# Optimization experiments

Hardware: AMD Instinct MI355X
Metric: run time of the kernel (lower is better)

The kernel has to match this reference:

```python
import jax, jax.numpy as jnp
import numpy as np

B, T, C = 2, 2048, 1024
H = 16
D = C // H  # head_size = 64
EPS = 1e-5


def setup_inputs() -> dict:
    key = jax.random.key(0)
    ks = jax.random.split(key, 16)
    s = lambda fan_in: fan_in ** -0.5
    return {
        "x": jax.random.normal(ks[0], (B, T, C), jnp.float32),
        "Wq": jax.random.normal(ks[1], (H, C, D), jnp.float32) * s(C),
        "Wk": jax.random.normal(ks[2], (H, C, D), jnp.float32) * s(C),
        "Wv": jax.random.normal(ks[3], (H, C, D), jnp.float32) * s(C),
        "Wproj": jax.random.normal(ks[4], (C, C), jnp.float32) * s(C),
        "bproj": jnp.zeros((C,), jnp.float32),
        "W1": jax.random.normal(ks[5], (C, 4 * C), jnp.float32) * s(C),
        "b1": jnp.zeros((4 * C,), jnp.float32),
        "W2": jax.random.normal(ks[6], (4 * C, C), jnp.float32) * s(4 * C),
        "b2": jnp.zeros((C,), jnp.float32),
        "ln1_g": jnp.ones((C,), jnp.float32),
        "ln1_b": jnp.zeros((C,), jnp.float32),
        "ln2_g": jnp.ones((C,), jnp.float32),
        "ln2_b": jnp.zeros((C,), jnp.float32),
    }


def _layernorm(x, g, b):
    mu = jnp.mean(x, axis=-1, keepdims=True)
    var = jnp.mean(jnp.square(x - mu), axis=-1, keepdims=True)
    return (x - mu) * jax.lax.rsqrt(var + EPS) * g + b


def _block(x, Wq, Wk, Wv, Wproj, bproj, W1, b1, W2, b2,
           ln1_g, ln1_b, ln2_g, ln2_b):
    # --- multi-head causal self-attention (pre-LN) ---
    h = _layernorm(x, ln1_g, ln1_b)
    q = jnp.einsum("btc,hcd->bhtd", h, Wq)
    k = jnp.einsum("btc,hcd->bhtd", h, Wk)
    v = jnp.einsum("btc,hcd->bhtd", h, Wv)
    scores = jnp.einsum("bhtd,bhsd->bhts", q, k) * (D ** -0.5)  # [B,H,T,T]
    causal = jnp.tril(jnp.ones((T, T), bool))
    scores = jnp.where(causal, scores, -jnp.inf)
    att = jax.nn.softmax(scores, axis=-1)
    out = jnp.einsum("bhts,bhsd->bhtd", att, v)  # [B,H,T,D]
    out = out.transpose(0, 2, 1, 3).reshape(B, T, H * D)  # concat heads
    x = x + out @ Wproj + bproj
    # --- feed-forward ---
    h2 = _layernorm(x, ln2_g, ln2_b)
    ff = jax.nn.relu(h2 @ W1 + b1) @ W2 + b2
    return x + ff


def reference(x, Wq, Wk, Wv, Wproj, bproj, W1, b1, W2, b2,
              ln1_g, ln1_b, ln2_g, ln2_b):
    return _block(x, Wq, Wk, Wv, Wproj, bproj, W1, b1, W2, b2,
                  ln1_g, ln1_b, ln2_g, ln2_b)
```

## Files before the change

### kernel.cpp

```cpp
#include <hip/hip_runtime.h>

typedef __bf16 bf16x8 __attribute__((ext_vector_type(8)));
typedef float  f32x4  __attribute__((ext_vector_type(4)));

union U8 { bf16x8 v; __bf16 e[8]; unsigned short u[8]; };

__device__ __forceinline__ unsigned short f2bf(float f) {
  unsigned int u = __float_as_uint(f);
  unsigned int r = (u + 0x7FFFu + ((u >> 16) & 1u)) >> 16;
  return (unsigned short)r;
}

__device__ __forceinline__ void async16(const void* g, void* l) {
  __builtin_amdgcn_global_load_lds(
      (__attribute__((address_space(1))) void*)(g),
      (__attribute__((address_space(3))) void*)(l), 16, 0, 0);
}

__device__ __forceinline__ void block_barrier() {
  asm volatile("" ::: "memory");
  __builtin_amdgcn_sched_barrier(0);
  __builtin_amdgcn_s_barrier();
  __builtin_amdgcn_sched_barrier(0);
  asm volatile("" ::: "memory");
}

__global__ __launch_bounds__(256) void transpose_w(
    const float* __restrict__ in, unsigned short* __restrict__ out,
    int R, int Cc) {
  __shared__ float tile[32][33];
  const int batch = blockIdx.z;
  const float* ip = in + (size_t)batch * R * Cc;
  unsigned short* op = out + (size_t)batch * R * Cc;
  const int c0 = blockIdx.x * 32, r0 = blockIdx.y * 32;
  const int tx = threadIdx.x, ty = threadIdx.y;
#pragma unroll
  for (int i = 0; i < 32; i += 8)
    tile[ty + i][tx] = ip[(size_t)(r0 + ty + i) * Cc + c0 + tx];
  __syncthreads();
#pragma unroll
  for (int i = 0; i < 32; i += 8)
    op[(size_t)(c0 + ty + i) * R + r0 + tx] = f2bf(tile[tx][ty + i]);
}

__global__ __launch_bounds__(256) void ln_kernel(
    const float* __restrict__ x, const float* __restrict__ g,
    const float* __restrict__ bta, unsigned short* __restrict__ out) {
  const int C = 1024;
  const int row = blockIdx.x, tid = threadIdx.x;
  const float4 v = ((const float4*)(x + (size_t)row * C))[tid];
  float s  = v.x + v.y + v.z + v.w;
  float ss = v.x * v.x + v.y * v.y + v.z * v.z + v.w * v.w;
#pragma unroll
  for (int off = 32; off > 0; off >>= 1) {
    s  += __shfl_down(s, off);
    ss += __shfl_down(ss, off);
  }
  __shared__ float r0[4], r1[4];
  const int wave = tid >> 6, lane = tid & 63;
  if (lane == 0) { r0[wave] = s; r1[wave] = ss; }
  __syncthreads();
  s  = r0[0] + r0[1] + r0[2] + r0[3];
  ss = r1[0] + r1[1] + r1[2] + r1[3];
  const float mu   = s * (1.0f / C);
  const float var  = ss * (1.0f / C) - mu * mu;
  const float rstd = rsqrtf(var + 1e-5f);
  const float4 gv = ((const float4*)g)[tid];
  const float4 bv = ((const float4*)bta)[tid];
  ushort4 o;
  o.x = f2bf((v.x - mu) * rstd * gv.x + bv.x);
  o.y = f2bf((v.y - mu) * rstd * gv.y + bv.y);
  o.z = f2bf((v.z - mu) * rstd * gv.z + bv.z);
  o.w = f2bf((v.w - mu) * rstd * gv.w + bv.w);
  ((ushort4*)(out + (size_t)row * C))[tid] = o;
}

__global__ __launch_bounds__(256, 2) void gemm_lat2(
    const unsigned short* __restrict__ A, const unsigned short* __restrict__ BT,
    float* __restrict__ Cout, const float* __restrict__ bias,
    const float* __restrict__ resid, int M, int N, int K) {
  __shared__ __align__(16) unsigned short As[3][8192];
  __shared__ __align__(16) unsigned short Bs[3][4096];
  const int tid = threadIdx.x;
  const int lane = tid & 63, wave = tid >> 6;
  const int wm = wave >> 1, wn = wave & 1;
  const int lr = lane & 15, lg = lane >> 4;

  const int nwg = gridDim.x;
  const int cpx = nwg >> 3;
  const int swz = ((int)blockIdx.x & 7) * cpx + ((int)blockIdx.x >> 3);
  const int Nt = N >> 6;
  const int g4 = swz / (4 * Nt);
  const int rem = swz - g4 * 4 * Nt;
  const int m0 = (g4 * 4 + (rem & 3)) << 7;
  const int n0 = (rem >> 2) << 6;

  const int srow = tid >> 3;
  const int sc = ((tid & 7) ^ (srow & 7)) << 3;
  const unsigned short* Ag = A + (size_t)(m0 + srow) * K + sc;
  const unsigned short* Bg = BT + (size_t)(n0 + srow) * K + sc;
  const size_t rskip = (size_t)32 * K;

  f32x4 acc[4][2] = {};
  const int nkt = K >> 6;

#define STG(T, B)                                                          \
  {                                                                        \
    const int kt_ = (T) << 6;                                              \
    _Pragma("unroll")                                                      \
    for (int j = 0; j < 4; ++j)                                            \
      async16(Ag + kt_ + (size_t)j * rskip, &As[B][j * 2048 + tid * 8]);   \
    async16(Bg + kt_, &Bs[B][tid * 8]);                                    \
    async16(Bg + kt_ + rskip, &Bs[B][2048 + tid * 8]);                     \
  }

  STG(0, 0);
  STG(1, 1);

  for (int t = 0; t < nkt; ++t) {
    const int buf = t % 3;
    if (t + 1 < nkt) asm volatile("s_waitcnt vmcnt(6)" ::: "memory");
    else             asm volatile("s_waitcnt vmcnt(0)" ::: "memory");
    block_barrier();
    if (t + 2 < nkt) {
      int sb = buf + 2; if (sb >= 3) sb -= 3;
      STG(t + 2, sb);
    }
#pragma unroll
    for (int kh = 0; kh < 2; ++kh) {
      const int kc = ((kh * 4 + lg) ^ (lr & 7)) << 3;
      bf16x8 afr[4], bfr[2];
#pragma unroll
      for (int fm = 0; fm < 4; fm++)
        afr[fm] = *(const bf16x8*)&As[buf][(wm * 64 + fm * 16 + lr) * 64 + kc];
#pragma unroll
      for (int fn = 0; fn < 2; fn++)
        bfr[fn] = *(const bf16x8*)&Bs[buf][(wn * 32 + fn * 16 + lr) * 64 + kc];
#pragma unroll
      for (int fm = 0; fm < 4; fm++)
#pragma unroll
        for (int fn = 0; fn < 2; fn++)
          acc[fm][fn] = __builtin_amdgcn_mfma_f32_16x16x32_bf16(
              afr[fm], bfr[fn], acc[fm][fn], 0, 0, 0);
    }
  }
#undef STG

#pragma unroll
  for (int fn = 0; fn < 2; fn++) {
    const int col = n0 + wn * 32 + fn * 16 + lr;
    const float bv = bias[col];
#pragma unroll
    for (int fm = 0; fm < 4; fm++) {
      const int row0 = m0 + wm * 64 + fm * 16 + lg * 4;
#pragma unroll
      for (int r = 0; r < 4; r++) {
        const size_t idx = (size_t)(row0 + r) * N + col;
        Cout[idx] = acc[fm][fn][r] + bv + resid[idx];
      }
    }
  }
}

template <int EPI>
__global__ __launch_bounds__(512, 2) void gemm8p(
    const unsigned short* __restrict__ A, const unsigned short* __restrict__ BT,
    void* __restrict__ Cout, void* __restrict__ Cout2,
    const float* __restrict__ bias, int M, int N, int K) {
  __shared__ __align__(16) unsigned short As[2][2][8192];
  __shared__ __align__(16) unsigned short Bs[2][2][8192];
  const int tid = threadIdx.x;
  const int lane = tid & 63;
  const int wave = tid >> 6;
  const int wm = wave >> 2, wn = wave & 3;
  const int lr = lane & 15, lg = lane >> 4;

  const int nwg = gridDim.x;
  const int cpx = nwg >> 3;
  const int swz = ((int)blockIdx.x & 7) * cpx + ((int)blockIdx.x >> 3);
  const int Nt = N >> 8;
  const int g4 = swz / (4 * Nt);
  const int rem = swz - g4 * 4 * Nt;
  const int m0 = (g4 * 4 + (rem & 3)) << 8;
  const int n0 = (rem >> 2) << 8;

  const int srow = tid >> 2;
  const int scg = ((tid & 3) ^ ((srow >> 1) & 3)) << 3;
  const unsigned short* Ag = A + (size_t)(m0 + srow) * K + scg;
  const unsigned short* Bg = BT + (size_t)(n0 + srow) * K + scg;
  const size_t rskip = (size_t)128 * K;
  const int l8 = tid * 8;

  const int kch = (lg ^ ((lr >> 1) & 3)) << 3;

  f32x4 acc[8][4] = {};
  bf16x8 afr[4], bfr[4];
  const int nkt = K >> 6;

  async16(Ag, &As[0][0][l8]);            async16(Ag + rskip, &As[0][0][l8 + 4096]);
  async16(Bg, &Bs[0][0][l8]);            async16(Bg + rskip, &Bs[0][0][l8 + 4096]);
  async16(Ag + 32, &As[0][1][l8]);       async16(Ag + 32 + rskip, &As[0][1][l8 + 4096]);
  async16(Bg + 32, &Bs[0][1][l8]);       async16(Bg + 32 + rskip, &Bs[0][1][l8 + 4096]);
  async16(Ag + 64, &As[1][0][l8]);       async16(Ag + 64 + rskip, &As[1][0][l8 + 4096]);
  async16(Bg + 64, &Bs[1][0][l8]);       async16(Bg + 64 + rskip, &Bs[1][0][l8 + 4096]);
  asm volatile("s_waitcnt vmcnt(4)" ::: "memory");
  block_barrier();

  for (int t = 0; t < nkt; ++t) {
    const int buf = t & 1, nbuf = buf ^ 1;
    const int kt1 = (t + 1) << 6, kt2 = (t + 2) << 6;
    const bool s1 = (t + 1 < nkt), s2 = (t + 2 < nkt);

#pragma unroll
    for (int fm = 0; fm < 4; fm++)
      afr[fm] = *(const bf16x8*)&As[buf][0][(wm * 128 + fm * 16 + lr) * 32 + kch];
#pragma unroll
    for (int fn = 0; fn < 4; fn++)
      bfr[fn] = *(const bf16x8*)&Bs[buf][0][(wn * 64 + fn * 16 + lr) * 32 + kch];
    if (s1) {
      async16(Ag + kt1 + 32, &As[nbuf][1][l8]);
      async16(Ag + kt1 + 32 + rskip, &As[nbuf][1][l8 + 4096]);
    }
    block_barrier();
    __builtin_amdgcn_s_setprio(1);
#pragma unroll
    for (int fm = 0; fm < 4; fm++)
#pragma unroll
      for (int fn = 0; fn < 4; fn++)
        acc[fm][fn] = __builtin_amdgcn_mfma_f32_16x16x32_bf16(afr[fm], bfr[fn], acc[fm][fn], 0, 0, 0);
    __builtin_amdgcn_s_setprio(0);
    block_barrier();

#pragma unroll
    for (int fm = 0; fm < 4; fm++)
      afr[fm] = *(const bf16x8*)&As[buf][0][(wm * 128 + 64 + fm * 16 + lr) * 32 + kch];
    if (s1) {
      async16(Bg + kt1 + 32, &Bs[nbuf][1][l8]);
      async16(Bg + kt1 + 32 + rskip, &Bs[nbuf][1][l8 + 4096]);
    }
    block_barrier();
    __builtin_amdgcn_s_setprio(1);
#pragma unroll
    for (int fm = 0; fm < 4; fm++)
#pragma unroll
      for (int fn = 0; fn < 4; fn++)
        acc[4 + fm][fn] = __builtin_amdgcn_mfma_f32_16x16x32_bf16(afr[fm], bfr[fn], acc[4 + fm][fn], 0, 0, 0);
    __builtin_amdgcn_s_setprio(0);
    block_barrier();

#pragma unroll
    for (int fm = 0; fm < 4; fm++)
      afr[fm] = *(const bf16x8*)&As[buf][1][(wm * 128 + fm * 16 + lr) * 32 + kch];
#pragma unroll
    for (int fn = 0; fn < 4; fn++)
      bfr[fn] = *(const bf16x8*)&Bs[buf][1][(wn * 64 + fn * 16 + lr) * 32 + kch];
    if (s2) {
      async16(Ag + kt2, &As[buf][0][l8]);
      async16(Ag + kt2 + rskip, &As[buf][0][l8 + 4096]);
    }
    block_barrier();
    __builtin_amdgcn_s_setprio(1);
#pragma unroll
    for (int fm = 0; fm < 4; fm++)
#pragma unroll
      for (int fn = 0; fn < 4; fn++)
        acc[fm][fn] = __builtin_amdgcn_mfma_f32_16x16x32_bf16(afr[fm], bfr[fn], acc[fm][fn], 0, 0, 0);
    __builtin_amdgcn_s_setprio(0);
    block_barrier();

#pragma unroll
    for (int fm = 0; fm < 4; fm++)
      afr[fm] = *(const bf16x8*)&As[buf][1][(wm * 128 + 64 + fm * 16 + lr) * 32 + kch];
    if (s2) {
      async16(Bg + kt2, &Bs[buf][0][l8]);
      async16(Bg + kt2 + rskip, &Bs[buf][0][l8 + 4096]);
    }
    block_barrier();
    __builtin_amdgcn_s_setprio(1);
#pragma unroll
    for (int fm = 0; fm < 4; fm++)
#pragma unroll
      for (int fn = 0; fn < 4; fn++)
        acc[4 + fm][fn] = __builtin_amdgcn_mfma_f32_16x16x32_bf16(afr[fm], bfr[fn], acc[4 + fm][fn], 0, 0, 0);
    __builtin_amdgcn_s_setprio(0);
    if (s2) asm volatile("s_waitcnt vmcnt(4)" ::: "memory");
    else    asm volatile("s_waitcnt vmcnt(0)" ::: "memory");
    block_barrier();
  }

#pragma unroll
  for (int fn = 0; fn < 4; fn++) {
    const int col = n0 + wn * 64 + fn * 16 + lr;
    float bv = 0.0f;
    if (EPI == 2) bv = bias[col];
#pragma unroll
    for (int fm = 0; fm < 8; fm++) {
      const int row0 = m0 + wm * 128 + fm * 16 + lg * 4;
      if (EPI == 2) {
#pragma unroll
        for (int r = 0; r < 4; r++)
          ((unsigned short*)Cout)[(size_t)(row0 + r) * N + col] =
              f2bf(fmaxf(acc[fm][fn][r] + bv, 0.0f));
      } else {
        if (col < 2048) {
#pragma unroll
          for (int r = 0; r < 4; r++)
            ((unsigned short*)Cout)[(size_t)(row0 + r) * 2048 + col] =
                f2bf(acc[fm][fn][r]);
        } else {
          ushort4 ov;
          ov.x = f2bf(acc[fm][fn][0]);
          ov.y = f2bf(acc[fm][fn][1]);
          ov.z = f2bf(acc[fm][fn][2]);
          ov.w = f2bf(acc[fm][fn][3]);
          *(ushort4*)((unsigned short*)Cout2 + (size_t)(col - 2048) * 4096 + row0) = ov;
        }
      }
    }
  }
}

__global__ __launch_bounds__(256) void attn_kernel(
    const unsigned short* __restrict__ qk, const unsigned short* __restrict__ vT,
    unsigned short* __restrict__ o) {
  const int T = 2048, C = 1024, QKS = 2048;
  const int tid = threadIdx.x;
  const int wave = tid >> 6, lane = tid & 63;
  const int lr = lane & 15, lg = lane >> 4;
  const int b = blockIdx.y >> 4, hh = blockIdx.y & 15;
  const size_t rowb = (size_t)b * T * QKS;
  const int qcol = hh * 64;
  const int kcol = 1024 + hh * 64;
  const int vrow0 = hh * 64;
  const size_t bT = (size_t)b * T;
  const int swe = (lr & 7) << 3;

  __shared__ __align__(16) unsigned short Ks[2][64 * 64];
  __shared__ __align__(16) unsigned short Vs[2][64 * 64];
  __shared__ __align__(16) unsigned short Ps[4][16][72];

  const int rw = tid >> 3;
  const int c8 = ((tid & 7) ^ (rw & 7)) << 3;

#pragma unroll 1
  for (int pass = 0; pass < 2; ++pass) {
    const int qt = (pass == 0) ? (int)blockIdx.x : (31 - (int)blockIdx.x);
    const int qbase = qt * 64 + wave * 16;
    const int trow = qbase + lr;

    U8 qf[2];
#pragma unroll
    for (int j = 0; j < 2; j++)
      qf[j].v = *(const bf16x8*)(qk + rowb + (size_t)trow * QKS + qcol + j * 32 + lg * 8);
    asm volatile("s_waitcnt vmcnt(0)" ::: "memory");

    async16(qk + rowb + (size_t)rw * QKS + kcol + c8, Ks[0] + tid * 8);
    async16(qk + rowb + (size_t)(32 + rw) * QKS + kcol + c8, Ks[0] + 2048 + tid * 8);
    async16(vT + (size_t)(vrow0 + rw) * 4096 + bT + c8, Vs[0] + tid * 8);
    async16(vT + (size_t)(vrow0 + 32 + rw) * 4096 + bT + c8, Vs[0] + 2048 + tid * 8);

    f32x4 oa[4] = {};
    float mrun = -1e30f, lsum = 0.0f;
    int cur = 0;

    for (int sb = 0; sb <= qt; ++sb) {
      if (sb < qt) {
        const int s1 = (sb + 1) * 64;
        const int nb = cur ^ 1;
        async16(qk + rowb + (size_t)(s1 + rw) * QKS + kcol + c8, Ks[nb] + tid * 8);
        async16(qk + rowb + (size_t)(s1 + 32 + rw) * QKS + kcol + c8, Ks[nb] + 2048 + tid * 8);
        async16(vT + (size_t)(vrow0 + rw) * 4096 + bT + s1 + c8, Vs[nb] + tid * 8);
        async16(vT + (size_t)(vrow0 + 32 + rw) * 4096 + bT + s1 + c8, Vs[nb] + 2048 + tid * 8);
        asm volatile("s_waitcnt vmcnt(4)" ::: "memory");
      } else {
        asm volatile("s_waitcnt vmcnt(0)" ::: "memory");
      }
      block_barrier();

      const unsigned short* Kc = Ks[cur];
      const unsigned short* Vc = Vs[cur];
      const int s0 = sb * 64;

      f32x4 sa[4] = {};
#pragma unroll
      for (int j = 0; j < 2; j++) {
#pragma unroll
        for (int mf = 0; mf < 4; mf++) {
          U8 kf;
          kf.v = *(const bf16x8*)(Kc + (mf * 16 + lr) * 64 + ((j * 32 + lg * 8) ^ swe));
          sa[mf] = __builtin_amdgcn_mfma_f32_16x16x32_bf16(kf.v, qf[j].v, sa[mf], 0, 0, 0);
        }
      }
      float sv[16];
#pragma unroll
      for (int mf = 0; mf < 4; mf++)
#pragma unroll
        for (int r = 0; r < 4; r++) sv[mf * 4 + r] = sa[mf][r] * 0.125f;

      if (sb == qt) {
#pragma unroll
        for (int mf = 0; mf < 4; mf++)
#pragma unroll
          for (int r = 0; r < 4; r++)
            if (s0 + mf * 16 + lg * 4 + r > trow) sv[mf * 4 + r] = -1e30f;
      }

      float tm = sv[0];
#pragma unroll
      for (int i = 1; i < 16; i++) tm = fmaxf(tm, sv[i]);
      tm = fmaxf(tm, __shfl_xor(tm, 16));
      tm = fmaxf(tm, __shfl_xor(tm, 32));

      if (!__all(tm <= mrun + 8.0f)) {
        const float mn = fmaxf(mrun, tm);
        const float corr = __expf(mrun - mn);
        lsum *= corr;
#pragma unroll
        for (int c = 0; c < 4; c++)
#pragma unroll
          for (int r = 0; r < 4; r++) oa[c][r] *= corr;
        mrun = mn;
      }

      float rs = 0.0f;
#pragma unroll
      for (int i = 0; i < 16; i++) {
        sv[i] = __expf(sv[i] - mrun);
        rs += sv[i];
      }
      rs += __shfl_xor(rs, 16);
      rs += __shfl_xor(rs, 32);
      lsum += rs;

#pragma unroll
      for (int mf = 0; mf < 4; mf++) {
        ushort4 w;
        w.x = f2bf(sv[mf * 4 + 0]);
        w.y = f2bf(sv[mf * 4 + 1]);
        w.z = f2bf(sv[mf * 4 + 2]);
        w.w = f2bf(sv[mf * 4 + 3]);
        *(ushort4*)&Ps[wave][lr][mf * 16 + lg * 4] = w;
      }
      asm volatile("" ::: "memory");
      U8 pb[2];
      pb[0].v = *(const bf16x8*)&Ps[wave][lr][lg * 8];
      pb[1].v = *(const bf16x8*)&Ps[wave][lr][32 + lg * 8];
      asm volatile("" ::: "memory");

#pragma unroll
      for (int c = 0; c < 4; c++) {
#pragma unroll
        for (int ks = 0; ks < 2; ks++) {
          U8 vf;
          vf.v = *(const bf16x8*)(Vc + (c * 16 + lr) * 64 + ((ks * 32 + lg * 8) ^ swe));
          oa[c] = __builtin_amdgcn_mfma_f32_16x16x32_bf16(vf.v, pb[ks].v, oa[c], 0, 0, 0);
        }
      }

      block_barrier();
      cur ^= 1;
    }

    const float inv = 1.0f / lsum;
#pragma unroll
    for (int c = 0; c < 4; c++) {
      ushort4 ov;
      ov.x = f2bf(oa[c][0] * inv);
      ov.y = f2bf(oa[c][1] * inv);
      ov.z = f2bf(oa[c][2] * inv);
      ov.w = f2bf(oa[c][3] * inv);
      *(ushort4*)(o + (size_t)(bT + trow) * C + hh * 64 + c * 16 + lg * 4) = ov;
    }
  }
}

extern "C" void kernel_launch(void* const* d_in, const int* in_sizes, int n_in,
                              void* d_out, int out_size, void* d_ws, size_t ws_size,
                              hipStream_t stream) {
  (void)in_sizes; (void)n_in; (void)out_size; (void)ws_size;
  const int T = 2048, C = 1024, M = 2 * T, C4 = 4 * C;

  const float* x     = (const float*)d_in[0];
  const float* Wq    = (const float*)d_in[1];
  const float* Wk    = (const float*)d_in[2];
  const float* Wv    = (const float*)d_in[3];
  const float* Wproj = (const float*)d_in[4];
  const float* bproj = (const float*)d_in[5];
  const float* W1    = (const float*)d_in[6];
  const float* b1    = (const float*)d_in[7];
  const float* W2    = (const float*)d_in[8];
  const float* b2    = (const float*)d_in[9];
  const float* ln1g  = (const float*)d_in[10];
  const float* ln1b  = (const float*)d_in[11];
  const float* ln2g  = (const float*)d_in[12];
  const float* ln2b  = (const float*)d_in[13];
  float* out = (float*)d_out;

  char* ws = (char*)d_ws;
  const size_t MBy = (size_t)1 << 20;
  unsigned short* WqkvT = (unsigned short*)(ws + 0 * MBy);
  unsigned short* WqT = WqkvT;
  unsigned short* WkT = WqkvT + 1024 * 1024;
  unsigned short* WvT = WqkvT + 2048 * 1024;
  unsigned short* WpT = (unsigned short*)(ws + 6 * MBy);
  unsigned short* W1T = (unsigned short*)(ws + 8 * MBy);
  unsigned short* W2T = (unsigned short*)(ws + 16 * MBy);
  unsigned short* h   = (unsigned short*)(ws + 24 * MBy);
  unsigned short* qkb = (unsigned short*)(ws + 32 * MBy);
  unsigned short* vTb = (unsigned short*)(ws + 48 * MBy);
  unsigned short* att = (unsigned short*)(ws + 56 * MBy);
  float*          x1  = (float*)(ws + 64 * MBy);
  unsigned short* h2  = att;
  unsigned short* ff1 = h;

  const dim3 tb(32, 8);
  transpose_w<<<dim3(2, 32, 16), tb, 0, stream>>>(Wq, WqT, 1024, 64);
  transpose_w<<<dim3(2, 32, 16), tb, 0, stream>>>(Wk, WkT, 1024, 64);
  transpose_w<<<dim3(2, 32, 16), tb, 0, stream>>>(Wv, WvT, 1024, 64);
  transpose_w<<<dim3(32, 32, 1), tb, 0, stream>>>(Wproj, WpT, 1024, 1024);
  transpose_w<<<dim3(128, 32, 1), tb, 0, stream>>>(W1, W1T, 1024, 4096);
  transpose_w<<<dim3(32, 128, 1), tb, 0, stream>>>(W2, W2T, 4096, 1024);

  ln_kernel<<<M, 256, 0, stream>>>(x, ln1g, ln1b, h);

  gemm8p<4><<<192, 512, 0, stream>>>(h, WqkvT, qkb, vTb, nullptr, M, 3072, C);

  attn_kernel<<<dim3(16, 32), 256, 0, stream>>>(qkb, vTb, att);

  gemm_lat2<<<512, 256, 0, stream>>>(att, WpT, x1, bproj, x, M, C, C);

  ln_kernel<<<M, 256, 0, stream>>>(x1, ln2g, ln2b, h2);

  gemm8p<2><<<256, 512, 0, stream>>>(h2, W1T, ff1, nullptr, b1, M, C4, C);

  gemm_lat2<<<512, 256, 0, stream>>>(ff1, W2T, out, b2, x1, M, C, C4);
}
```

Before: 252.2 us.

## Replace LDS-staged GEMM with direct global-to-register double-buffered loads

The projection and FFN2 GEMM kernel stops staging A/B tiles through LDS with async loads and barriers. Each wave now loads its MFMA fragments straight from global memory into registers, using two register buffers so the loads for the next k-tile overlap the MFMAs on the current one. This removes the LDS traffic and block barriers, but each wave now fetches its own operand fragments with no sharing inside the workgroup. It also uses narrower, less coalesced global accesses and relies on L2/L1 to absorb the redundant reads.

```diff
diff --git a/kernel.cpp b/kernel.cpp
--- a/kernel.cpp
+++ b/kernel.cpp
@@ -75,12 +75,10 @@
   ((ushort4*)(out + (size_t)row * C))[tid] = o;
 }
 
-__global__ __launch_bounds__(256, 2) void gemm_lat2(
+__global__ __launch_bounds__(256, 2) void gemm_reg(
     const unsigned short* __restrict__ A, const unsigned short* __restrict__ BT,
     float* __restrict__ Cout, const float* __restrict__ bias,
     const float* __restrict__ resid, int M, int N, int K) {
-  __shared__ __align__(16) unsigned short As[3][8192];
-  __shared__ __align__(16) unsigned short Bs[3][4096];
   const int tid = threadIdx.x;
   const int lane = tid & 63, wave = tid >> 6;
   const int wm = wave >> 1, wn = wave & 1;
@@ -95,56 +93,72 @@
   const int m0 = (g4 * 4 + (rem & 3)) << 7;
   const int n0 = (rem >> 2) << 6;
 
-  const int srow = tid >> 3;
-  const int sc = ((tid & 7) ^ (srow & 7)) << 3;
-  const unsigned short* Ag = A + (size_t)(m0 + srow) * K + sc;
-  const unsigned short* Bg = BT + (size_t)(n0 + srow) * K + sc;
-  const size_t rskip = (size_t)32 * K;
-
+  const unsigned short* pa0 = A + (size_t)(m0 + wm * 64 +  0 + lr) * K + lg * 8;
+  const unsigned short* pa1 = A + (size_t)(m0 + wm * 64 + 16 + lr) * K + lg * 8;
+  const unsigned short* pa2 = A + (size_t)(m0 + wm * 64 + 32 + lr) * K + lg * 8;
+  const unsigned short* pa3 = A + (size_t)(m0 + wm * 64 + 48 + lr) * K + lg * 8;
+  const unsigned short* pb0 = BT + (size_t)(n0 + wn * 32 +  0 + lr) * K + lg * 8;
+  const unsigned short* pb1 = BT + (size_t)(n0 + wn * 32 + 16 + lr) * K + lg * 8;
+
+  bf16x8 a0[2][4], b0[2][2], a1[2][4], b1[2][2];
   f32x4 acc[4][2] = {};
-  const int nkt = K >> 6;
-
-#define STG(T, B)                                                          \
-  {                                                                        \
-    const int kt_ = (T) << 6;                                              \
-    _Pragma("unroll")                                                      \
-    for (int j = 0; j < 4; ++j)                                            \
-      async16(Ag + kt_ + (size_t)j * rskip, &As[B][j * 2048 + tid * 8]);   \
-    async16(Bg + kt_, &Bs[B][tid * 8]);                                    \
-    async16(Bg + kt_ + rskip, &Bs[B][2048 + tid * 8]);                     \
-  }
-
-  STG(0, 0);
-  STG(1, 1);
-
-  for (int t = 0; t < nkt; ++t) {
-    const int buf = t % 3;
-    if (t + 1 < nkt) asm volatile("s_waitcnt vmcnt(6)" ::: "memory");
-    else             asm volatile("s_waitcnt vmcnt(0)" ::: "memory");
-    block_barrier();
-    if (t + 2 < nkt) {
-      int sb = buf + 2; if (sb >= 3) sb -= 3;
-      STG(t + 2, sb);
-    }
-#pragma unroll
-    for (int kh = 0; kh < 2; ++kh) {
-      const int kc = ((kh * 4 + lg) ^ (lr & 7)) << 3;
-      bf16x8 afr[4], bfr[2];
-#pragma unroll
-      for (int fm = 0; fm < 4; fm++)
-        afr[fm] = *(const bf16x8*)&As[buf][(wm * 64 + fm * 16 + lr) * 64 + kc];
-#pragma unroll
-      for (int fn = 0; fn < 2; fn++)
-        bfr[fn] = *(const bf16x8*)&Bs[buf][(wn * 32 + fn * 16 + lr) * 64 + kc];
-#pragma unroll
-      for (int fm = 0; fm < 4; fm++)
-#pragma unroll
-        for (int fn = 0; fn < 2; fn++)
-          acc[fm][fn] = __builtin_amdgcn_mfma_f32_16x16x32_bf16(
-              afr[fm], bfr[fn], acc[fm][fn], 0, 0, 0);
-    }
-  }
-#undef STG
+
+#define LD_T0                                                     \
+  {                                                               \
+    _Pragma("unroll")                                             \
+    for (int kh = 0; kh < 2; kh++) {                              \
+      a0[kh][0] = *(const bf16x8*)(pa0 + kh * 32);                \
+      a0[kh][1] = *(const bf16x8*)(pa1 + kh * 32);                \
+      a0[kh][2] = *(const bf16x8*)(pa2 + kh * 32);                \
+      a0[kh][3] = *(const bf16x8*)(pa3 + kh * 32);                \
+      b0[kh][0] = *(const bf16x8*)(pb0 + kh * 32);                \
+      b0[kh][1] = *(const bf16x8*)(pb1 + kh * 32);                \
+    }                                                             \
+  }
+#define LD_T1                                                     \
+  {                                                               \
+    _Pragma("unroll")                                             \
+    for (int kh = 0; kh < 2; kh++) {                              \
+      a1[kh][0] = *(const bf16x8*)(pa0 + 64 + kh * 32);           \
+      a1[kh][1] = *(const bf16x8*)(pa1 + 64 + kh * 32);           \
+      a1[kh][2] = *(const bf16x8*)(pa2 + 64 + kh * 32);           \
+      a1[kh][3] = *(const bf16x8*)(pa3 + 64 + kh * 32);           \
+      b1[kh][0] = *(const bf16x8*)(pb0 + 64 + kh * 32);           \
+      b1[kh][1] = *(const bf16x8*)(pb1 + 64 + kh * 32);           \
+    }                                                             \
+  }
+#define ADV { pa0 += 128; pa1 += 128; pa2 += 128; pa3 += 128; pb0 += 128; pb1 += 128; }
+#define FMAS(aa, bb)                                                        \
+  {                                                                         \
+    _Pragma("unroll")                                                       \
+    for (int kh = 0; kh < 2; kh++)                                          \
+      _Pragma("unroll")                                                     \
+      for (int fm = 0; fm < 4; fm++)                                        \
+        _Pragma("unroll")                                                   \
+        for (int fn = 0; fn < 2; fn++)                                      \
+          acc[fm][fn] = __builtin_amdgcn_mfma_f32_16x16x32_bf16(            \
+              aa[kh][fm], bb[kh][fn], acc[fm][fn], 0, 0, 0);                \
+  }
+
+  const int niter = K >> 7;
+  LD_T0;
+  LD_T1;
+  ADV;
+#pragma unroll 1
+  for (int i = 0; i < niter - 1; ++i) {
+    FMAS(a0, b0);
+    LD_T0;
+    FMAS(a1, b1);
+    LD_T1;
+    ADV;
+  }
+  FMAS(a0, b0);
+  FMAS(a1, b1);
+
+#undef LD_T0
+#undef LD_T1
+#undef ADV
+#undef FMAS
 
 #pragma unroll
   for (int fn = 0; fn < 2; fn++) {
@@ -527,11 +541,11 @@
 
   attn_kernel<<<dim3(16, 32), 256, 0, stream>>>(qkb, vTb, att);
 
-  gemm_lat2<<<512, 256, 0, stream>>>(att, WpT, x1, bproj, x, M, C, C);
+  gemm_reg<<<512, 256, 0, stream>>>(att, WpT, x1, bproj, x, M, C, C);
 
   ln_kernel<<<M, 256, 0, stream>>>(x1, ln2g, ln2b, h2);
 
   gemm8p<2><<<256, 512, 0, stream>>>(h2, W1T, ff1, nullptr, b1, M, C4, C);
 
-  gemm_lat2<<<512, 256, 0, stream>>>(ff1, W2T, out, b2, x1, M, C, C4);
-}
+  gemm_reg<<<512, 256, 0, stream>>>(ff1, W2T, out, b2, x1, M, C, C4);
+}
```

After: 391.0 us. +55.0%, slower.

## Split-K the N=1024 GEMMs into two partials plus a fused reduce kernel

Applied to the files above, without the earlier changes.

The projection and FF2 GEMMs now split K in half across twice as many workgroups. Each half writes an fp32 partial tile, and a new elementwise kernel sums the two partials with the bias and residual. The GEMM also drops from a 3-stage to a 2-stage LDS pipeline, with a second barrier per iteration and launch bounds raised to 3 waves per SIMD. The aim is more parallelism and occupancy on the 256 CUs. In exchange it adds extra global traffic for the partials and an extra kernel launch, and workspace buffers are reused as partial storage.

```diff
diff --git a/kernel.cpp b/kernel.cpp
--- a/kernel.cpp
+++ b/kernel.cpp
@@ -75,12 +75,12 @@
   ((ushort4*)(out + (size_t)row * C))[tid] = o;
 }
 
-__global__ __launch_bounds__(256, 2) void gemm_lat2(
+__global__ __launch_bounds__(256, 3) void gemm_sk(
     const unsigned short* __restrict__ A, const unsigned short* __restrict__ BT,
-    float* __restrict__ Cout, const float* __restrict__ bias,
-    const float* __restrict__ resid, int M, int N, int K) {
-  __shared__ __align__(16) unsigned short As[3][8192];
-  __shared__ __align__(16) unsigned short Bs[3][4096];
+    float* __restrict__ P0, float* __restrict__ P1,
+    int M, int N, int K) {
+  __shared__ __align__(16) unsigned short As[2][8192];
+  __shared__ __align__(16) unsigned short Bs[2][4096];
   const int tid = threadIdx.x;
   const int lane = tid & 63, wave = tid >> 6;
   const int wm = wave >> 1, wn = wave & 1;
@@ -89,20 +89,23 @@
   const int nwg = gridDim.x;
   const int cpx = nwg >> 3;
   const int swz = ((int)blockIdx.x & 7) * cpx + ((int)blockIdx.x >> 3);
+  const int tile = swz >> 1, ks = swz & 1;
   const int Nt = N >> 6;
-  const int g4 = swz / (4 * Nt);
-  const int rem = swz - g4 * 4 * Nt;
+  const int g4 = tile / (4 * Nt);
+  const int rem = tile - g4 * 4 * Nt;
   const int m0 = (g4 * 4 + (rem & 3)) << 7;
   const int n0 = (rem >> 2) << 6;
+  const int K2 = K >> 1;
+  const int k0 = ks * K2;
 
   const int srow = tid >> 3;
   const int sc = ((tid & 7) ^ (srow & 7)) << 3;
-  const unsigned short* Ag = A + (size_t)(m0 + srow) * K + sc;
-  const unsigned short* Bg = BT + (size_t)(n0 + srow) * K + sc;
+  const unsigned short* Ag = A + (size_t)(m0 + srow) * K + k0 + sc;
+  const unsigned short* Bg = BT + (size_t)(n0 + srow) * K + k0 + sc;
   const size_t rskip = (size_t)32 * K;
 
   f32x4 acc[4][2] = {};
-  const int nkt = K >> 6;
+  const int nkt = K2 >> 6;
 
 #define STG(T, B)                                                          \
   {                                                                        \
@@ -115,17 +118,16 @@
   }
 
   STG(0, 0);
-  STG(1, 1);
 
   for (int t = 0; t < nkt; ++t) {
-    const int buf = t % 3;
-    if (t + 1 < nkt) asm volatile("s_waitcnt vmcnt(6)" ::: "memory");
-    else             asm volatile("s_waitcnt vmcnt(0)" ::: "memory");
-    block_barrier();
-    if (t + 2 < nkt) {
-      int sb = buf + 2; if (sb >= 3) sb -= 3;
-      STG(t + 2, sb);
-    }
+    const int buf = t & 1;
+    if (t + 1 < nkt) {
+      STG(t + 1, buf ^ 1);
+      asm volatile("s_waitcnt vmcnt(6)" ::: "memory");
+    } else {
+      asm volatile("s_waitcnt vmcnt(0)" ::: "memory");
+    }
+    block_barrier();
 #pragma unroll
     for (int kh = 0; kh < 2; ++kh) {
       const int kc = ((kh * 4 + lg) ^ (lr & 7)) << 3;
@@ -143,22 +145,40 @@
           acc[fm][fn] = __builtin_amdgcn_mfma_f32_16x16x32_bf16(
               afr[fm], bfr[fn], acc[fm][fn], 0, 0, 0);
     }
+    block_barrier();
   }
 #undef STG
 
+  float* P = ks ? P1 : P0;
 #pragma unroll
   for (int fn = 0; fn < 2; fn++) {
     const int col = n0 + wn * 32 + fn * 16 + lr;
-    const float bv = bias[col];
 #pragma unroll
     for (int fm = 0; fm < 4; fm++) {
       const int row0 = m0 + wm * 64 + fm * 16 + lg * 4;
 #pragma unroll
-      for (int r = 0; r < 4; r++) {
-        const size_t idx = (size_t)(row0 + r) * N + col;
-        Cout[idx] = acc[fm][fn][r] + bv + resid[idx];
-      }
-    }
+      for (int r = 0; r < 4; r++)
+        P[(size_t)(row0 + r) * N + col] = acc[fm][fn][r];
+    }
+  }
+}
+
+__global__ __launch_bounds__(256) void reduce_add(
+    const float* __restrict__ p0, const float* __restrict__ p1,
+    const float* __restrict__ bias, const float* __restrict__ resid,
+    float* __restrict__ out, int n4) {
+  const int stride = gridDim.x * 256;
+  for (int i = blockIdx.x * 256 + threadIdx.x; i < n4; i += stride) {
+    const float4 a = ((const float4*)p0)[i];
+    const float4 b = ((const float4*)p1)[i];
+    const float4 c = ((const float4*)resid)[i];
+    const float4 bv = ((const float4*)bias)[i & 255];
+    float4 o;
+    o.x = a.x + b.x + c.x + bv.x;
+    o.y = a.y + b.y + c.y + bv.y;
+    o.z = a.z + b.z + c.z + bv.z;
+    o.w = a.w + b.w + c.w + bv.w;
+    ((float4*)out)[i] = o;
   }
 }
 
@@ -509,9 +529,13 @@
   unsigned short* qkb = (unsigned short*)(ws + 32 * MBy);
   unsigned short* vTb = (unsigned short*)(ws + 48 * MBy);
   unsigned short* att = (unsigned short*)(ws + 56 * MBy);
-  float*          x1  = (float*)(ws + 64 * MBy);
+  float* projP0 = (float*)(ws + 24 * MBy);
+  float* projP1 = (float*)(ws + 40 * MBy);
+  float* x1     = out;
   unsigned short* h2  = att;
   unsigned short* ff1 = h;
+  float* ffP0 = (float*)(ws + 64 * MBy);
+  float* ffP1 = (float*)(ws + 0 * MBy);
 
   const dim3 tb(32, 8);
   transpose_w<<<dim3(2, 32, 16), tb, 0, stream>>>(Wq, WqT, 1024, 64);
@@ -527,11 +551,13 @@
 
   attn_kernel<<<dim3(16, 32), 256, 0, stream>>>(qkb, vTb, att);
 
-  gemm_lat2<<<512, 256, 0, stream>>>(att, WpT, x1, bproj, x, M, C, C);
+  gemm_sk<<<1024, 256, 0, stream>>>(att, WpT, projP0, projP1, M, C, C);
+  reduce_add<<<2048, 256, 0, stream>>>(projP0, projP1, bproj, x, x1, M * C / 4);
 
   ln_kernel<<<M, 256, 0, stream>>>(x1, ln2g, ln2b, h2);
 
   gemm8p<2><<<256, 512, 0, stream>>>(h2, W1T, ff1, nullptr, b1, M, C4, C);
 
-  gemm_lat2<<<512, 256, 0, stream>>>(ff1, W2T, out, b2, x1, M, C, C4);
-}
+  gemm_sk<<<1024, 256, 0, stream>>>(ff1, W2T, ffP0, ffP1, M, C, C4);
+  reduce_add<<<2048, 256, 0, stream>>>(ffP0, ffP1, b2, x1, out, M * C / 4);
+}
```

Measured after the change: 272.7 us. 8.1% more time.
